# Kernel optimization log

Measured on AMD Instinct MI355X. Metric: run time of the kernel, lower is better.

Reference implementation:

```python
import jax, jax.numpy as jnp
import numpy as np

N_HEAD = 32
HEAD_DIM = 32  # must equal N_HEAD due to the module's einsum index reuse
N_EMBD = N_HEAD * HEAD_DIM
VOCAB = 32000
B, T = 2, 64
TEMP_MIN = 0.1


def setup_inputs() -> dict:
    key = jax.random.key(0)
    ks = jax.random.split(key, 8)
    inv = 1.0 / np.sqrt(HEAD_DIM)
    return {
        "x": jax.random.normal(ks[0], (B, T, N_EMBD), dtype=jnp.float32),
        "vocab_emb": jax.random.normal(ks[1], (VOCAB, N_EMBD), dtype=jnp.float32) * 0.02,
        "W_ffn": jax.random.normal(ks[2], (HEAD_DIM, HEAD_DIM), dtype=jnp.float32) * inv,
        "b_ffn": jnp.zeros((HEAD_DIM,), dtype=jnp.float32),
        "temps": jnp.ones((N_HEAD,), dtype=jnp.float32),
        "W_ref": jax.random.normal(ks[3], (HEAD_DIM, HEAD_DIM), dtype=jnp.float32) * inv,
        "b_ref": jnp.zeros((HEAD_DIM,), dtype=jnp.float32),
        "W_gate": jax.random.normal(ks[4], (HEAD_DIM, HEAD_DIM), dtype=jnp.float32) * inv,
        "b_gate": jnp.zeros((HEAD_DIM,), dtype=jnp.float32),
    }


def reference(x, vocab_emb, W_ffn, b_ffn, temps, W_ref, b_ref, W_gate, b_gate):
    Bs, Ts, C = x.shape
    # per-head channel decomposition: (B*T, n_head, head_dim)
    xc = x.reshape(Bs * Ts, N_HEAD, HEAD_DIM)
    # channel_ffns: shared Linear over the head_dim axis (torch Linear: x @ W.T + b)
    ffn = jnp.einsum('bnh,dh->bnd', xc, W_ffn) + b_ffn
    # vocab channels: (n_head, vocab, head_dim)
    vc = vocab_emb.reshape(VOCAB, N_HEAD, HEAD_DIM).transpose(1, 0, 2)
    temps_c = jnp.clip(temps, TEMP_MIN, None)[None, :, None]

    def vocab_project(q):
        # faithful to torch: einsum('bnh,hvd->bnv') contracts q's head_dim
        # against vc's HEAD axis and sums over d as well (requires head_dim == n_head)
        logits = jnp.einsum('bnh,hvd->bnv', q, vc)
        w = jax.nn.softmax(logits / temps_c, axis=-1)  # (B*T, n_head, vocab)
        return jnp.einsum('bnv,hvd->bnh', w, vc)

    vocab_out = vocab_project(ffn)  # (B*T, n_head, head_dim)

    # refinement stage (use_vocab_refinement=True)
    refinement = jnp.tanh(jnp.einsum('bnh,dh->bnd', xc, W_ref) + b_ref)
    gate = jax.nn.sigmoid(jnp.einsum('bnh,dh->bnd', xc, W_gate) + b_gate)
    refined = vocab_out * (1.0 - gate) + refinement * gate
    vocab_out = vocab_project(refined)

    # dropout p=0 (eval) -> identity
    return vocab_out.reshape(Bs, Ts, C)
```

## Files before the change

### kernel.cpp

```cpp
#include <hip/hip_runtime.h>
#include <hip/hip_bf16.h>
#include <cstdint>

typedef unsigned int uint;
typedef unsigned short ushort_t;

typedef __attribute__((ext_vector_type(8))) short short8;
typedef __attribute__((ext_vector_type(4))) short short4_t;
typedef __attribute__((ext_vector_type(4))) float float4_t;

#define NEMBD 1024
#define VOCAB 32000
#define NQ 4096
#define CHUNKS 1000
#define LOG2E 1.4426950408889634f

__device__ __forceinline__ ushort_t f2bf_rne(float f) {
    uint u = __float_as_uint(f);
    u += 0x7fffu + ((u >> 16) & 1u);
    return (ushort_t)(u >> 16);
}

__global__ void k_build_st(const float* __restrict__ ve, ushort_t* __restrict__ ST) {
    int v = blockIdx.x;
    int t = threadIdx.x;
    const float4* row = (const float4*)(ve + (size_t)v * NEMBD);
    float4 f = row[t];
    float s = f.x + f.y + f.z + f.w;
    s += __shfl_down(s, 4, 8);
    s += __shfl_down(s, 2, 8);
    s += __shfl_down(s, 1, 8);
    if ((t & 7) == 0) ST[v * 32 + (t >> 3)] = f2bf_rne(s);
}

__global__ void k_build_s2(const ushort_t* __restrict__ ST, ushort_t* __restrict__ S2) {
    int tid = blockIdx.x * 256 + threadIdx.x;
    int l = tid & 63, f = (tid >> 6) & 1, c = tid >> 7;
    int quad = l >> 4, lo = l & 15;
    uint w[4];
    #pragma unroll
    for (int t = 0; t < 2; t++) {
        #pragma unroll
        for (int jj = 0; jj < 2; jj++) {
            ushort_t v0 = ST[(c * 32 + t * 16 + quad * 4 + jj * 2 + 0) * 32 + f * 16 + lo];
            ushort_t v1 = ST[(c * 32 + t * 16 + quad * 4 + jj * 2 + 1) * 32 + f * 16 + lo];
            w[t * 2 + jj] = (uint)v0 | ((uint)v1 << 16);
        }
    }
    uint4* dst = (uint4*)S2;
    dst[tid] = make_uint4(w[0], w[1], w[2], w[3]);
}

__global__ void k_q1(const float* __restrict__ x, const float* __restrict__ W,
                     const float* __restrict__ b, const float* __restrict__ temps,
                     float* __restrict__ q1) {
    int tid = blockIdx.x * 256 + threadIdx.x;
    int i = tid >> 5, d = tid & 31, n = i & 31;
    const float* xr = x + i * 32;
    float s = b[d];
    #pragma unroll
    for (int h = 0; h < 32; h++) s += xr[h] * W[d * 32 + h];
    q1[tid] = s * (LOG2E / fmaxf(temps[n], 0.1f));
}

__launch_bounds__(512)
__global__ void k_proj(const ushort_t* __restrict__ ST, const ushort_t* __restrict__ S2,
                       const float* __restrict__ q, float* __restrict__ pN,
                       float* __restrict__ pD) {
    int g = blockIdx.x >> 3, p = blockIdx.x & 7;
    int wave = threadIdx.x >> 6, lane = threadIdx.x & 63;
    int quad = lane >> 4, lo = lane & 15;

    short8 qf[8];
    #pragma unroll
    for (int s = 0; s < 8; s++) {
        const float* qp = q + ((g * 128 + s * 16 + lo) * 32 + quad * 8);
        short8 v;
        #pragma unroll
        for (int j = 0; j < 8; j++) v[j] = (short)f2bf_rne(qp[j]);
        qf[s] = v;
    }

    float4_t pv0[8], pv1[8], dq[8];
    #pragma unroll
    for (int s = 0; s < 8; s++) {
        pv0[s] = (float4_t){0.f, 0.f, 0.f, 0.f};
        pv1[s] = (float4_t){0.f, 0.f, 0.f, 0.f};
        dq[s]  = (float4_t){0.f, 0.f, 0.f, 0.f};
    }
    const short4_t ones = {(short)0x3F80, (short)0x3F80, (short)0x3F80, (short)0x3F80};
    const float4_t zero4 = (float4_t){0.f, 0.f, 0.f, 0.f};

    for (int k = wave; k < 125; k += 8) {
        int c = p * 125 + k;
        const ushort_t* pa = ST + ((c * 32 + lo) * 32 + quad * 8);
        short8 a0 = *(const short8*)pa;
        short8 a1 = *(const short8*)(pa + 512);
        const ushort_t* pb = S2 + ((size_t)(c * 2) * 64 + lane) * 8;
        short8 sb0 = *(const short8*)pb;
        short8 sb1 = *(const short8*)(pb + 512);
        short4_t b00 = {sb0[0], sb0[1], sb0[2], sb0[3]};
        short4_t b01 = {sb0[4], sb0[5], sb0[6], sb0[7]};
        short4_t b10 = {sb1[0], sb1[1], sb1[2], sb1[3]};
        short4_t b11 = {sb1[4], sb1[5], sb1[6], sb1[7]};

        #pragma unroll
        for (int s = 0; s < 8; s++) {
            float4_t l0 = __builtin_amdgcn_mfma_f32_16x16x32_bf16(a0, qf[s], zero4, 0, 0, 0);
            float4_t l1 = __builtin_amdgcn_mfma_f32_16x16x32_bf16(a1, qf[s], zero4, 0, 0, 0);
            float e0 = exp2f(l0[0]), e1 = exp2f(l0[1]), e2 = exp2f(l0[2]), e3 = exp2f(l0[3]);
            float f0 = exp2f(l1[0]), f1 = exp2f(l1[1]), f2 = exp2f(l1[2]), f3 = exp2f(l1[3]);
            uint u0 = __builtin_amdgcn_perm(__float_as_uint(e1), __float_as_uint(e0), 0x07060302u);
            uint u1 = __builtin_amdgcn_perm(__float_as_uint(e3), __float_as_uint(e2), 0x07060302u);
            uint u2 = __builtin_amdgcn_perm(__float_as_uint(f1), __float_as_uint(f0), 0x07060302u);
            uint u3 = __builtin_amdgcn_perm(__float_as_uint(f3), __float_as_uint(f2), 0x07060302u);
            union { uint u[2]; short4_t s4; } c0, c1;
            c0.u[0] = u0; c0.u[1] = u1;
            c1.u[0] = u2; c1.u[1] = u3;
            short4_t P0 = c0.s4, P1 = c1.s4;
            pv0[s] = __builtin_amdgcn_mfma_f32_16x16x16bf16_1k(P0, b00, pv0[s], 0, 0, 0);
            pv0[s] = __builtin_amdgcn_mfma_f32_16x16x16bf16_1k(P1, b01, pv0[s], 0, 0, 0);
            pv1[s] = __builtin_amdgcn_mfma_f32_16x16x16bf16_1k(P0, b10, pv1[s], 0, 0, 0);
            pv1[s] = __builtin_amdgcn_mfma_f32_16x16x16bf16_1k(P1, b11, pv1[s], 0, 0, 0);
            dq[s] = __builtin_amdgcn_mfma_f32_16x16x16bf16_1k(P0, ones, dq[s], 0, 0, 0);
            dq[s] = __builtin_amdgcn_mfma_f32_16x16x16bf16_1k(P1, ones, dq[s], 0, 0, 0);
        }
    }

    __shared__ float red[8][64][12];
    int gp = blockIdx.x;
    for (int s = 0; s < 8; s++) {
        #pragma unroll
        for (int r = 0; r < 4; r++) {
            red[wave][lane][r]     = pv0[s][r];
            red[wave][lane][4 + r] = pv1[s][r];
            red[wave][lane][8 + r] = dq[s][r];
        }
        __syncthreads();
        if (wave == 0) {
            #pragma unroll
            for (int r = 0; r < 4; r++) {
                float n0 = 0.f, n1 = 0.f, dd = 0.f;
                #pragma unroll
                for (int w = 0; w < 8; w++) {
                    n0 += red[w][lane][r];
                    n1 += red[w][lane][4 + r];
                    dd += red[w][lane][8 + r];
                }
                int ql = s * 16 + quad * 4 + r;
                pN[(size_t)gp * 4096 + ql * 32 + lo]      = n0;
                pN[(size_t)gp * 4096 + ql * 32 + 16 + lo] = n1;
                if (lo == 0) pD[gp * 128 + ql] = dd;
            }
        }
        __syncthreads();
    }
}

__global__ void k_refine(const float* __restrict__ pN, const float* __restrict__ pD,
                         const float* __restrict__ x,
                         const float* __restrict__ Wr, const float* __restrict__ br,
                         const float* __restrict__ Wg, const float* __restrict__ bg,
                         const float* __restrict__ temps, float* __restrict__ q2) {
    int tid = blockIdx.x * 256 + threadIdx.x;
    int i = tid >> 5, h = tid & 31, n = i & 31;
    int g = i >> 7, ql = i & 127;
    float N = 0.f, D = 0.f;
    #pragma unroll
    for (int p = 0; p < 8; p++) {
        N += pN[((size_t)(g * 8 + p)) * 4096 + ql * 32 + h];
        D += pD[(g * 8 + p) * 128 + ql];
    }
    float vo = N / D;
    const float* xr = x + i * 32;
    float sr = br[h], sg = bg[h];
    #pragma unroll
    for (int h2 = 0; h2 < 32; h2++) {
        sr += xr[h2] * Wr[h * 32 + h2];
        sg += xr[h2] * Wg[h * 32 + h2];
    }
    float ref  = tanhf(sr);
    float gate = 1.f / (1.f + __expf(-sg));
    float refined = vo * (1.f - gate) + ref * gate;
    q2[tid] = refined * (LOG2E / fmaxf(temps[n], 0.1f));
}

__global__ void k_final(const float* __restrict__ pN, const float* __restrict__ pD,
                        float* __restrict__ out) {
    int tid = blockIdx.x * 256 + threadIdx.x;
    int i = tid >> 5, h = tid & 31;
    int g = i >> 7, ql = i & 127;
    float N = 0.f, D = 0.f;
    #pragma unroll
    for (int p = 0; p < 8; p++) {
        N += pN[((size_t)(g * 8 + p)) * 4096 + ql * 32 + h];
        D += pD[(g * 8 + p) * 128 + ql];
    }
    out[tid] = N / D;
}

extern "C" void kernel_launch(void* const* d_in, const int* in_sizes, int n_in,
                              void* d_out, int out_size, void* d_ws, size_t ws_size,
                              hipStream_t stream) {
    const float* x     = (const float*)d_in[0];
    const float* ve    = (const float*)d_in[1];
    const float* Wf    = (const float*)d_in[2];
    const float* bf    = (const float*)d_in[3];
    const float* temps = (const float*)d_in[4];
    const float* Wr    = (const float*)d_in[5];
    const float* br    = (const float*)d_in[6];
    const float* Wg    = (const float*)d_in[7];
    const float* bg    = (const float*)d_in[8];
    float* out = (float*)d_out;

    char* ws = (char*)d_ws;
    ushort_t* ST = (ushort_t*)ws;
    ushort_t* S2 = (ushort_t*)(ws + 2048000);
    float* q1 = (float*)(ws + 4096000);
    float* q2 = (float*)(ws + 4096000 + 524288);
    float* pN = (float*)(ws + 4096000 + 2 * 524288);
    float* pD = (float*)(ws + 4096000 + 2 * 524288 + 4194304);

    k_build_st<<<dim3(VOCAB), dim3(256), 0, stream>>>(ve, ST);
    k_build_s2<<<dim3(500), dim3(256), 0, stream>>>(ST, S2);
    k_q1<<<dim3(512), dim3(256), 0, stream>>>(x, Wf, bf, temps, q1);
    k_proj<<<dim3(256), dim3(512), 0, stream>>>(ST, S2, q1, pN, pD);
    k_refine<<<dim3(512), dim3(256), 0, stream>>>(pN, pD, x, Wr, br, Wg, bg, temps, q2);
    k_proj<<<dim3(256), dim3(512), 0, stream>>>(ST, S2, q2, pN, pD);
    k_final<<<dim3(512), dim3(256), 0, stream>>>(pN, pD, out);
}
```

Before: 315.4 us.

## Repartition projection across more blocks and compute softmax denominator on VALU

The projection kernel now runs 1024 blocks of 256 threads, each covering 64 queries and a sixteenth of the vocabulary, where before it ran 256 blocks of 512 threads covering 128 queries and an eighth. It drops the two ones-matrix MFMAs per step that built the denominator, and instead sums the bf16-rounded exponentials with scalar adds plus a cross-lane shuffle. Queries are stored in bf16 by the producing kernels, and exp2f is replaced by the hardware exp2 intrinsic. The aim is better occupancy, fewer MFMA issues and fewer qf/accumulator registers, at the cost of twice as many partials for the reduction kernels to read and more VALU work.

Result: faster. 266.4 us (-15.5%).

```diff
diff --git a/kernel.cpp b/kernel.cpp
--- a/kernel.cpp
+++ b/kernel.cpp
@@ -11,8 +11,6 @@
 
 #define NEMBD 1024
 #define VOCAB 32000
-#define NQ 4096
-#define CHUNKS 1000
 #define LOG2E 1.4426950408889634f
 
 __device__ __forceinline__ ushort_t f2bf_rne(float f) {
@@ -53,50 +51,45 @@
 
 __global__ void k_q1(const float* __restrict__ x, const float* __restrict__ W,
                      const float* __restrict__ b, const float* __restrict__ temps,
-                     float* __restrict__ q1) {
+                     ushort_t* __restrict__ q1) {
     int tid = blockIdx.x * 256 + threadIdx.x;
     int i = tid >> 5, d = tid & 31, n = i & 31;
     const float* xr = x + i * 32;
     float s = b[d];
     #pragma unroll
     for (int h = 0; h < 32; h++) s += xr[h] * W[d * 32 + h];
-    q1[tid] = s * (LOG2E / fmaxf(temps[n], 0.1f));
-}
-
-__launch_bounds__(512)
+    q1[tid] = f2bf_rne(s * (LOG2E / fmaxf(temps[n], 0.1f)));
+}
+
+__launch_bounds__(256, 4)
 __global__ void k_proj(const ushort_t* __restrict__ ST, const ushort_t* __restrict__ S2,
-                       const float* __restrict__ q, float* __restrict__ pN,
+                       const ushort_t* __restrict__ q, float* __restrict__ pN,
                        float* __restrict__ pD) {
-    int g = blockIdx.x >> 3, p = blockIdx.x & 7;
+    int g = blockIdx.x >> 4, p = blockIdx.x & 15;
     int wave = threadIdx.x >> 6, lane = threadIdx.x & 63;
     int quad = lane >> 4, lo = lane & 15;
 
-    short8 qf[8];
-    #pragma unroll
-    for (int s = 0; s < 8; s++) {
-        const float* qp = q + ((g * 128 + s * 16 + lo) * 32 + quad * 8);
-        short8 v;
-        #pragma unroll
-        for (int j = 0; j < 8; j++) v[j] = (short)f2bf_rne(qp[j]);
-        qf[s] = v;
-    }
-
-    float4_t pv0[8], pv1[8], dq[8];
-    #pragma unroll
-    for (int s = 0; s < 8; s++) {
+    short8 qf[4];
+    #pragma unroll
+    for (int s = 0; s < 4; s++)
+        qf[s] = *(const short8*)(q + ((g * 64 + s * 16 + lo) * 32 + quad * 8));
+
+    float4_t pv0[4], pv1[4];
+    float dsum[4];
+    #pragma unroll
+    for (int s = 0; s < 4; s++) {
         pv0[s] = (float4_t){0.f, 0.f, 0.f, 0.f};
         pv1[s] = (float4_t){0.f, 0.f, 0.f, 0.f};
-        dq[s]  = (float4_t){0.f, 0.f, 0.f, 0.f};
-    }
-    const short4_t ones = {(short)0x3F80, (short)0x3F80, (short)0x3F80, (short)0x3F80};
+        dsum[s] = 0.f;
+    }
     const float4_t zero4 = (float4_t){0.f, 0.f, 0.f, 0.f};
 
-    for (int k = wave; k < 125; k += 8) {
-        int c = p * 125 + k;
-        const ushort_t* pa = ST + ((c * 32 + lo) * 32 + quad * 8);
+    int start = (p * 125) >> 1, end = ((p + 1) * 125) >> 1;
+    for (int k = start + wave; k < end; k += 4) {
+        const ushort_t* pa = ST + ((k * 32 + lo) * 32 + quad * 8);
         short8 a0 = *(const short8*)pa;
         short8 a1 = *(const short8*)(pa + 512);
-        const ushort_t* pb = S2 + ((size_t)(c * 2) * 64 + lane) * 8;
+        const ushort_t* pb = S2 + ((size_t)(k * 2) * 64 + lane) * 8;
         short8 sb0 = *(const short8*)pb;
         short8 sb1 = *(const short8*)(pb + 512);
         short4_t b00 = {sb0[0], sb0[1], sb0[2], sb0[3]};
@@ -105,15 +98,25 @@
         short4_t b11 = {sb1[4], sb1[5], sb1[6], sb1[7]};
 
         #pragma unroll
-        for (int s = 0; s < 8; s++) {
+        for (int s = 0; s < 4; s++) {
             float4_t l0 = __builtin_amdgcn_mfma_f32_16x16x32_bf16(a0, qf[s], zero4, 0, 0, 0);
             float4_t l1 = __builtin_amdgcn_mfma_f32_16x16x32_bf16(a1, qf[s], zero4, 0, 0, 0);
-            float e0 = exp2f(l0[0]), e1 = exp2f(l0[1]), e2 = exp2f(l0[2]), e3 = exp2f(l0[3]);
-            float f0 = exp2f(l1[0]), f1 = exp2f(l1[1]), f2 = exp2f(l1[2]), f3 = exp2f(l1[3]);
+            float e0 = __builtin_amdgcn_exp2f(l0[0]);
+            float e1 = __builtin_amdgcn_exp2f(l0[1]);
+            float e2 = __builtin_amdgcn_exp2f(l0[2]);
+            float e3 = __builtin_amdgcn_exp2f(l0[3]);
+            float f0 = __builtin_amdgcn_exp2f(l1[0]);
+            float f1 = __builtin_amdgcn_exp2f(l1[1]);
+            float f2 = __builtin_amdgcn_exp2f(l1[2]);
+            float f3 = __builtin_amdgcn_exp2f(l1[3]);
             uint u0 = __builtin_amdgcn_perm(__float_as_uint(e1), __float_as_uint(e0), 0x07060302u);
             uint u1 = __builtin_amdgcn_perm(__float_as_uint(e3), __float_as_uint(e2), 0x07060302u);
             uint u2 = __builtin_amdgcn_perm(__float_as_uint(f1), __float_as_uint(f0), 0x07060302u);
             uint u3 = __builtin_amdgcn_perm(__float_as_uint(f3), __float_as_uint(f2), 0x07060302u);
+            dsum[s] += __uint_as_float(u0 << 16) + __uint_as_float(u0 & 0xffff0000u)
+                     + __uint_as_float(u1 << 16) + __uint_as_float(u1 & 0xffff0000u)
+                     + __uint_as_float(u2 << 16) + __uint_as_float(u2 & 0xffff0000u)
+                     + __uint_as_float(u3 << 16) + __uint_as_float(u3 & 0xffff0000u);
             union { uint u[2]; short4_t s4; } c0, c1;
             c0.u[0] = u0; c0.u[1] = u1;
             c1.u[0] = u2; c1.u[1] = u3;
@@ -122,35 +125,41 @@
             pv0[s] = __builtin_amdgcn_mfma_f32_16x16x16bf16_1k(P1, b01, pv0[s], 0, 0, 0);
             pv1[s] = __builtin_amdgcn_mfma_f32_16x16x16bf16_1k(P0, b10, pv1[s], 0, 0, 0);
             pv1[s] = __builtin_amdgcn_mfma_f32_16x16x16bf16_1k(P1, b11, pv1[s], 0, 0, 0);
-            dq[s] = __builtin_amdgcn_mfma_f32_16x16x16bf16_1k(P0, ones, dq[s], 0, 0, 0);
-            dq[s] = __builtin_amdgcn_mfma_f32_16x16x16bf16_1k(P1, ones, dq[s], 0, 0, 0);
-        }
-    }
-
-    __shared__ float red[8][64][12];
+        }
+    }
+
+    #pragma unroll
+    for (int s = 0; s < 4; s++) {
+        dsum[s] += __shfl_xor(dsum[s], 16, 64);
+        dsum[s] += __shfl_xor(dsum[s], 32, 64);
+    }
+
+    __shared__ float red[4][64][9];
     int gp = blockIdx.x;
-    for (int s = 0; s < 8; s++) {
+    for (int s = 0; s < 4; s++) {
         #pragma unroll
         for (int r = 0; r < 4; r++) {
             red[wave][lane][r]     = pv0[s][r];
             red[wave][lane][4 + r] = pv1[s][r];
-            red[wave][lane][8 + r] = dq[s][r];
-        }
+        }
+        red[wave][lane][8] = dsum[s];
         __syncthreads();
         if (wave == 0) {
             #pragma unroll
             for (int r = 0; r < 4; r++) {
-                float n0 = 0.f, n1 = 0.f, dd = 0.f;
+                float n0 = 0.f, n1 = 0.f;
                 #pragma unroll
-                for (int w = 0; w < 8; w++) {
+                for (int w = 0; w < 4; w++) {
                     n0 += red[w][lane][r];
                     n1 += red[w][lane][4 + r];
-                    dd += red[w][lane][8 + r];
                 }
                 int ql = s * 16 + quad * 4 + r;
-                pN[(size_t)gp * 4096 + ql * 32 + lo]      = n0;
-                pN[(size_t)gp * 4096 + ql * 32 + 16 + lo] = n1;
-                if (lo == 0) pD[gp * 128 + ql] = dd;
+                pN[((size_t)gp * 64 + ql) * 32 + lo]      = n0;
+                pN[((size_t)gp * 64 + ql) * 32 + 16 + lo] = n1;
+            }
+            if (quad == 0) {
+                float dd = red[0][lane][8] + red[1][lane][8] + red[2][lane][8] + red[3][lane][8];
+                pD[gp * 64 + s * 16 + lo] = dd;
             }
         }
         __syncthreads();
@@ -161,15 +170,15 @@
                          const float* __restrict__ x,
                          const float* __restrict__ Wr, const float* __restrict__ br,
                          const float* __restrict__ Wg, const float* __restrict__ bg,
-                         const float* __restrict__ temps, float* __restrict__ q2) {
+                         const float* __restrict__ temps, ushort_t* __restrict__ q2) {
     int tid = blockIdx.x * 256 + threadIdx.x;
     int i = tid >> 5, h = tid & 31, n = i & 31;
-    int g = i >> 7, ql = i & 127;
+    int g = i >> 6, ql = i & 63;
     float N = 0.f, D = 0.f;
     #pragma unroll
-    for (int p = 0; p < 8; p++) {
-        N += pN[((size_t)(g * 8 + p)) * 4096 + ql * 32 + h];
-        D += pD[(g * 8 + p) * 128 + ql];
+    for (int p = 0; p < 16; p++) {
+        N += pN[((size_t)(g * 16 + p) * 64 + ql) * 32 + h];
+        D += pD[(g * 16 + p) * 64 + ql];
     }
     float vo = N / D;
     const float* xr = x + i * 32;
@@ -182,19 +191,19 @@
     float ref  = tanhf(sr);
     float gate = 1.f / (1.f + __expf(-sg));
     float refined = vo * (1.f - gate) + ref * gate;
-    q2[tid] = refined * (LOG2E / fmaxf(temps[n], 0.1f));
+    q2[tid] = f2bf_rne(refined * (LOG2E / fmaxf(temps[n], 0.1f)));
 }
 
 __global__ void k_final(const float* __restrict__ pN, const float* __restrict__ pD,
                         float* __restrict__ out) {
     int tid = blockIdx.x * 256 + threadIdx.x;
     int i = tid >> 5, h = tid & 31;
-    int g = i >> 7, ql = i & 127;
+    int g = i >> 6, ql = i & 63;
     float N = 0.f, D = 0.f;
     #pragma unroll
-    for (int p = 0; p < 8; p++) {
-        N += pN[((size_t)(g * 8 + p)) * 4096 + ql * 32 + h];
-        D += pD[(g * 8 + p) * 128 + ql];
+    for (int p = 0; p < 16; p++) {
+        N += pN[((size_t)(g * 16 + p) * 64 + ql) * 32 + h];
+        D += pD[(g * 16 + p) * 64 + ql];
     }
     out[tid] = N / D;
 }
@@ -216,16 +225,16 @@
     char* ws = (char*)d_ws;
     ushort_t* ST = (ushort_t*)ws;
     ushort_t* S2 = (ushort_t*)(ws + 2048000);
-    float* q1 = (float*)(ws + 4096000);
-    float* q2 = (float*)(ws + 4096000 + 524288);
-    float* pN = (float*)(ws + 4096000 + 2 * 524288);
-    float* pD = (float*)(ws + 4096000 + 2 * 524288 + 4194304);
+    ushort_t* q1 = (ushort_t*)(ws + 4096000);
+    ushort_t* q2 = (ushort_t*)(ws + 4096000 + 262144);
+    float* pN = (float*)(ws + 4096000 + 2 * 262144);
+    float* pD = (float*)(ws + 4096000 + 2 * 262144 + 8388608);
 
     k_build_st<<<dim3(VOCAB), dim3(256), 0, stream>>>(ve, ST);
     k_build_s2<<<dim3(500), dim3(256), 0, stream>>>(ST, S2);
     k_q1<<<dim3(512), dim3(256), 0, stream>>>(x, Wf, bf, temps, q1);
-    k_proj<<<dim3(256), dim3(512), 0, stream>>>(ST, S2, q1, pN, pD);
+    k_proj<<<dim3(1024), dim3(256), 0, stream>>>(ST, S2, q1, pN, pD);
     k_refine<<<dim3(512), dim3(256), 0, stream>>>(pN, pD, x, Wr, br, Wg, bg, temps, q2);
-    k_proj<<<dim3(256), dim3(512), 0, stream>>>(ST, S2, q2, pN, pD);
+    k_proj<<<dim3(1024), dim3(256), 0, stream>>>(ST, S2, q2, pN, pD);
     k_final<<<dim3(512), dim3(256), 0, stream>>>(pN, pD, out);
 }
```
